# Kernel tuning notes

Hardware: AMD Instinct MI355X
Metric: run time of the kernel (lower is better)

Reference implementation:

```python
import jax, jax.numpy as jnp
import numpy as np

NUM_LAYERS = 4
INPUT_SIZE = 80
D_MODEL = 512
NHEAD = 8
D_FF = 2048
B = 16
S_MAX = 512
LN_EPS = 1e-5


def setup_inputs() -> dict:
    key = jax.random.key(0)
    ks = jax.random.split(key, 16)
    L, D, F, I = NUM_LAYERS, D_MODEL, D_FF, INPUT_SIZE
    s = 0.02
    inp = {
        "x": jax.random.normal(ks[0], (B, S_MAX, I), dtype=jnp.float32),
        "lens": jax.random.randint(ks[1], (B,), S_MAX // 2, S_MAX + 1, dtype=jnp.int32),
        "We": jax.random.normal(ks[2], (D, I), jnp.float32) * s,
        "be": jnp.zeros((D,), jnp.float32),
        "Wqkv": jax.random.normal(ks[3], (L, 3 * D, D), jnp.float32) * s,
        "bqkv": jnp.zeros((L, 3 * D), jnp.float32),
        "Wo": jax.random.normal(ks[4], (L, D, D), jnp.float32) * s,
        "bo": jnp.zeros((L, D), jnp.float32),
        "ln1_g": jnp.ones((L, D), jnp.float32),
        "ln1_b": jnp.zeros((L, D), jnp.float32),
        "W1": jax.random.normal(ks[5], (L, F, D), jnp.float32) * s,
        "b1": jnp.zeros((L, F), jnp.float32),
        "W2": jax.random.normal(ks[6], (L, D, F), jnp.float32) * s,
        "b2": jnp.zeros((L, D), jnp.float32),
        "ln2_g": jnp.ones((L, D), jnp.float32),
        "ln2_b": jnp.zeros((L, D), jnp.float32),
    }
    return inp


def _layer_norm(x, g, b):
    m = jnp.mean(x, axis=-1, keepdims=True)
    v = jnp.mean(jnp.square(x - m), axis=-1, keepdims=True)
    return (x - m) * jax.lax.rsqrt(v + LN_EPS) * g + b


def _pos_encoding(S, D, dtype):
    pos = jnp.arange(S, dtype=jnp.float32)[:, None]
    div = jnp.exp(jnp.arange(0, D, 2, dtype=jnp.float32) * (-np.log(10000.0) / D))
    pe = jnp.zeros((S, D), jnp.float32)
    pe = pe.at[:, 0::2].set(jnp.sin(pos * div))
    pe = pe.at[:, 1::2].set(jnp.cos(pos * div))
    return pe.astype(dtype)


def _encoder_layer(h, key_mask, Wqkv, bqkv, Wo, bo, g1, b1_, W1, b1f, W2, b2f, g2, b2_):
    # h: [B,S,D], key_mask: [B,S] bool (True = valid). Post-norm (PyTorch default).
    Bq, S, D = h.shape
    dh = D // NHEAD
    qkv = jnp.einsum("bsd,ed->bse", h, Wqkv) + bqkv  # [B,S,3D]
    q, k, v = jnp.split(qkv, 3, axis=-1)
    q = q.reshape(Bq, S, NHEAD, dh).transpose(0, 2, 1, 3)
    k = k.reshape(Bq, S, NHEAD, dh).transpose(0, 2, 1, 3)
    v = v.reshape(Bq, S, NHEAD, dh).transpose(0, 2, 1, 3)
    scores = jnp.einsum("bhqd,bhkd->bhqk", q, k) / jnp.sqrt(jnp.asarray(dh, h.dtype))
    scores = jnp.where(key_mask[:, None, None, :], scores, jnp.asarray(-1e9, h.dtype))
    attn = jax.nn.softmax(scores, axis=-1)
    ctx = jnp.einsum("bhqk,bhkd->bhqd", attn, v)
    ctx = ctx.transpose(0, 2, 1, 3).reshape(Bq, S, D)
    attn_out = jnp.einsum("bsd,ed->bse", ctx, Wo) + bo
    h = _layer_norm(h + attn_out, g1, b1_)
    ff = jnp.einsum("bsf,df->bsd", jax.nn.relu(jnp.einsum("bsd,fd->bsf", h, W1) + b1f), W2) + b2f
    return _layer_norm(h + ff, g2, b2_)


def reference(x, lens, We, be, Wqkv, bqkv, Wo, bo, ln1_g, ln1_b, W1, b1, W2, b2, ln2_g, ln2_b):
    Bq, S, _ = x.shape
    D = We.shape[0]
    h = jnp.einsum("bsi,di->bsd", x, We) + be  # Linear embedding
    h = h + _pos_encoding(S, D, h.dtype)[None]
    key_mask = jnp.arange(S)[None, :] < lens[:, None]  # [B,S]
    for l in range(Wqkv.shape[0]):
        h = _encoder_layer(h, key_mask, Wqkv[l], bqkv[l], Wo[l], bo[l],
                           ln1_g[l], ln1_b[l], W1[l], b1[l], W2[l], b2[l],
                           ln2_g[l], ln2_b[l])
    pooled = jnp.sum(h * key_mask[..., None].astype(h.dtype), axis=1)
    pooled = pooled / lens[:, None].astype(h.dtype)  # mean over valid tokens
    return pooled, lens
```

## Files before the change

kernel.cpp:

```cpp
#include <hip/hip_runtime.h>
#include <math.h>

#define D_MODEL 512
#define NHEAD   8
#define DH      64
#define D_FF    2048
#define BATCH   16
#define SMAX    512
#define NTOK    (BATCH*SMAX)
#define NLAYER  4

constexpr int MODE_QK   = 1;
constexpr int MODE_VT   = 2;
constexpr int MODE_RELU = 3;
constexpr int MODE_PART = 4;

typedef __attribute__((ext_vector_type(8))) __bf16 bf16x8;
typedef __attribute__((ext_vector_type(4))) float  f32x4;
typedef __attribute__((ext_vector_type(8))) int    i32x8;
typedef unsigned char u8;

#define WSCALE_INV 0.03125f
#define QSCALE     0.18033688011112042f

__device__ __forceinline__ unsigned short f2bf(float f) {
  union { float f; unsigned u; } v; v.f = f;
  unsigned r = v.u + 0x7FFFu + ((v.u >> 16) & 1u);
  return (unsigned short)(r >> 16);
}
__device__ __forceinline__ float bf2f(unsigned short u) {
  union { unsigned u; float f; } v; v.u = ((unsigned)u) << 16; return v.f;
}
__device__ __forceinline__ int pk4(float a, float b, float c, float d) {
  int t = __builtin_amdgcn_cvt_pk_fp8_f32(a, b, 0, false);
  t = __builtin_amdgcn_cvt_pk_fp8_f32(c, d, t, true);
  return t;
}

__device__ __forceinline__ void gl_lds16(const unsigned short* g, unsigned short* l) {
  __builtin_amdgcn_global_load_lds(
      (const __attribute__((address_space(1))) unsigned int*)g,
      (__attribute__((address_space(3)))       unsigned int*)l, 16, 0, 0);
}
__device__ __forceinline__ void gl_lds16b(const u8* g, u8* l) {
  __builtin_amdgcn_global_load_lds(
      (const __attribute__((address_space(1))) unsigned int*)g,
      (__attribute__((address_space(3)))       unsigned int*)l, 16, 0, 0);
}

__device__ __forceinline__ i32x8 ldfrag(const u8* base, int row, int q) {
  const int rx = row & 7;
  const int4 lo = *(const int4*)(base + (row << 7) + ((((2*q)    ) ^ rx) << 4));
  const int4 hi = *(const int4*)(base + (row << 7) + ((((2*q) + 1) ^ rx) << 4));
  union { int4 p[2]; i32x8 v; } u;
  u.p[0] = lo; u.p[1] = hi;
  return u.v;
}

template<int MODE>
__global__ __launch_bounds__(256)
void gemm_fp8(const u8* __restrict__ A, const u8* __restrict__ Bw,
              const float* __restrict__ bias, u8* __restrict__ C8,
              unsigned short* __restrict__ Cb,
              unsigned short* __restrict__ qd, unsigned short* __restrict__ kd,
              const int* __restrict__ lens, int K, int CK, int N)
{
  const int lin = blockIdx.x + gridDim.x*(blockIdx.y + gridDim.y*blockIdx.z);
  int m0, n0, kz = 0;
  {
    m0 = (lin % gridDim.y) * 128;
    const int rest = lin / gridDim.y;
    n0 = (rest % gridDim.x) * 128;
    kz = rest / gridDim.x;
  }
  if ((m0 & 511) >= lens[m0 >> 9]) return;

  __shared__ __attribute__((aligned(16))) u8 As[2][16384];
  __shared__ __attribute__((aligned(16))) u8 Bs[2][16384];
  const int tid  = threadIdx.x;
  const int lane = tid & 63;
  const int w    = tid >> 6;
  const int wm   = (w & 1) * 64;
  const int wn   = (w >> 1) * 64;
  const int l15  = lane & 15, quad = lane >> 4;

  f32x4 acc[4][4] = {};

  const int sr  = tid >> 3;
  const int sch = ((tid & 7) ^ (sr & 7)) * 16;
  const u8* Ag = A  + (long)(m0 + sr) * K + kz*CK + sch;
  const u8* Bg = Bw + (long)(n0 + sr) * K + kz*CK + sch;
  const long rowskip = (long)32 * K;
  const int t16 = tid * 16;
  const int niter = CK >> 7;

  auto stage = [&](int t, int bix) {
    const u8* a_ = Ag + t*128;
    const u8* b_ = Bg + t*128;
#pragma unroll
    for (int s = 0; s < 4; s++) {
      gl_lds16b(a_ + s*rowskip, &As[bix][s*4096 + t16]);
      gl_lds16b(b_ + s*rowskip, &Bs[bix][s*4096 + t16]);
    }
  };

  stage(0, 0);
  stage(1, 1);

  for (int it = 0; it < niter; ++it) {
    if (it + 1 < niter)
      asm volatile("s_waitcnt vmcnt(8)\n\ts_barrier" ::: "memory");
    else
      asm volatile("s_waitcnt vmcnt(0)\n\ts_barrier" ::: "memory");

    const int cur = it & 1;
    const u8* Ac = &As[cur][0];
    const u8* Bc = &Bs[cur][0];

    i32x8 bfv[4];
#pragma unroll
    for (int j = 0; j < 4; j++)
      bfv[j] = ldfrag(Bc, wn + j*16 + l15, quad);
#pragma unroll
    for (int i = 0; i < 4; i++) {
      const i32x8 af = ldfrag(Ac, wm + i*16 + l15, quad);
#pragma unroll
      for (int j = 0; j < 4; j++)
        acc[i][j] = __builtin_amdgcn_mfma_scale_f32_16x16x128_f8f6f4(
            af, bfv[j], acc[i][j], 0, 0, 0, 0x7F7F7F7F, 0, 0x7F7F7F7F);
    }

    if (it + 2 < niter) {
      __syncthreads();
      stage(it + 2, cur);
    }
  }

  __syncthreads();
  const int rr8 = lane >> 3, ch8 = lane & 7;

  if (MODE == MODE_RELU) {
    float* epf = (float*)&As[0][0] + w * 1088;
#pragma unroll
    for (int i = 0; i < 4; i++) {
#pragma unroll
      for (int j = 0; j < 4; j++) {
        const float cbv = bias[n0 + wn + j*16 + l15];
#pragma unroll
        for (int r = 0; r < 4; r++)
          epf[(quad*4 + r)*68 + j*16 + l15] = fmaxf(acc[i][j][r]*WSCALE_INV + cbv, 0.f);
      }
      asm volatile("s_waitcnt lgkmcnt(0)" ::: "memory");
      const int row = lane >> 2, c16 = (lane & 3) * 16;
      const float* rp = epf + row*68 + c16;
      f32x4 f0 = *(const f32x4*)(rp + 0);
      f32x4 f1 = *(const f32x4*)(rp + 4);
      f32x4 f2 = *(const f32x4*)(rp + 8);
      f32x4 f3 = *(const f32x4*)(rp + 12);
      int4 o;
      o.x = pk4(f0.x, f0.y, f0.z, f0.w);
      o.y = pk4(f1.x, f1.y, f1.z, f1.w);
      o.z = pk4(f2.x, f2.y, f2.z, f2.w);
      o.w = pk4(f3.x, f3.y, f3.z, f3.w);
      const int mrow = m0 + wm + i*16 + row;
      *(int4*)&C8[(long)mrow*N + n0 + wn + c16] = o;
      asm volatile("s_waitcnt lgkmcnt(0)" ::: "memory");
    }
  } else {
    unsigned short* epi = (unsigned short*)&As[0][0] + w * 1152;
#pragma unroll
    for (int i = 0; i < 4; i++) {
#pragma unroll
      for (int j = 0; j < 4; j++) {
#pragma unroll
        for (int r = 0; r < 4; r++) {
          float v = acc[i][j][r] * WSCALE_INV;
          epi[(quad*4 + r)*72 + j*16 + l15] = f2bf(v);
        }
      }
      asm volatile("s_waitcnt lgkmcnt(0)" ::: "memory");
#pragma unroll
      for (int rs = 0; rs < 2; rs++) {
        const int row  = rs*8 + rr8;
        const int mrow = m0 + wm + i*16 + row;
        bf16x8 val = *(const bf16x8*)&epi[row*72 + ch8*8];
        *(bf16x8*)&Cb[((long)kz*NTOK + mrow)*N + n0 + wn + ch8*8] = val;
      }
      asm volatile("s_waitcnt lgkmcnt(0)" ::: "memory");
    }
  }
}

__global__ __launch_bounds__(256)
void gemm_qkv(const u8* __restrict__ h8, const u8* __restrict__ wq,
              const float* __restrict__ bqkv,
              unsigned short* __restrict__ qd, unsigned short* __restrict__ kd,
              unsigned short* __restrict__ vt_b,
              const int* __restrict__ lens)
{
  const int lin = blockIdx.x;
  const bool isVT = lin >= 512;
  int m0, n0;
  if (isVT) { const int idx = lin - 512; n0 = (idx & 63) * 128; m0 = (idx >> 6) * 128; }
  else      { m0 = (lin & 63) * 128;     n0 = (lin >> 6) * 128; }
  { const int tb = isVT ? n0 : m0;
    if ((tb & 511) >= lens[tb >> 9]) return; }

  const u8* Ap = isVT ? (wq + (long)2*D_MODEL*D_MODEL) : h8;
  const u8* Bp = isVT ? h8 : wq;

  __shared__ __attribute__((aligned(16))) u8 As[2][16384];
  __shared__ __attribute__((aligned(16))) u8 Bs[2][16384];
  const int tid  = threadIdx.x;
  const int lane = tid & 63;
  const int w    = tid >> 6;
  const int wm   = (w & 1) * 64;
  const int wn   = (w >> 1) * 64;
  const int l15  = lane & 15, quad = lane >> 4;

  f32x4 acc[4][4] = {};

  const int sr  = tid >> 3;
  const int sch = ((tid & 7) ^ (sr & 7)) * 16;
  const u8* Ag = Ap + (long)(m0 + sr) * 512 + sch;
  const u8* Bg = Bp + (long)(n0 + sr) * 512 + sch;
  const long rowskip = (long)32 * 512;
  const int t16 = tid * 16;

  auto stage = [&](int t, int bix) {
    const u8* a_ = Ag + t*128;
    const u8* b_ = Bg + t*128;
#pragma unroll
    for (int s = 0; s < 4; s++) {
      gl_lds16b(a_ + s*rowskip, &As[bix][s*4096 + t16]);
      gl_lds16b(b_ + s*rowskip, &Bs[bix][s*4096 + t16]);
    }
  };

  stage(0, 0);
  stage(1, 1);

#pragma unroll 1
  for (int it = 0; it < 4; ++it) {
    if (it + 1 < 4)
      asm volatile("s_waitcnt vmcnt(8)\n\ts_barrier" ::: "memory");
    else
      asm volatile("s_waitcnt vmcnt(0)\n\ts_barrier" ::: "memory");

    const int cur = it & 1;
    const u8* Ac = &As[cur][0];
    const u8* Bc = &Bs[cur][0];

    i32x8 bfv[4];
#pragma unroll
    for (int j = 0; j < 4; j++)
      bfv[j] = ldfrag(Bc, wn + j*16 + l15, quad);
#pragma unroll
    for (int i = 0; i < 4; i++) {
      const i32x8 af = ldfrag(Ac, wm + i*16 + l15, quad);
#pragma unroll
      for (int j = 0; j < 4; j++)
        acc[i][j] = __builtin_amdgcn_mfma_scale_f32_16x16x128_f8f6f4(
            af, bfv[j], acc[i][j], 0, 0, 0, 0x7F7F7F7F, 0, 0x7F7F7F7F);
    }

    if (it + 2 < 4) {
      __syncthreads();
      stage(it + 2, cur);
    }
  }

  __syncthreads();
  const int rr8 = lane >> 3, ch8 = lane & 7;
  unsigned short* epi = (unsigned short*)&As[0][0] + w * 1152;
  const bool isq = !isVT && (((n0 + wn) >> 9) == 0);
#pragma unroll
  for (int i = 0; i < 4; i++) {
    float rbv[4];
    if (isVT) {
#pragma unroll
      for (int r = 0; r < 4; r++) rbv[r] = bqkv[2*D_MODEL + m0 + wm + i*16 + quad*4 + r];
    }
#pragma unroll
    for (int j = 0; j < 4; j++) {
      float cbv = 0.f;
      if (!isVT) cbv = bqkv[n0 + wn + j*16 + l15];
#pragma unroll
      for (int r = 0; r < 4; r++) {
        float v = acc[i][j][r] * WSCALE_INV;
        if (!isVT) { v += cbv; if (isq) v *= QSCALE; }
        else       v += rbv[r];
        epi[(quad*4 + r)*72 + j*16 + l15] = f2bf(v);
      }
    }
    asm volatile("s_waitcnt lgkmcnt(0)" ::: "memory");
#pragma unroll
    for (int rs = 0; rs < 2; rs++) {
      const int row  = rs*8 + rr8;
      const int mrow = m0 + wm + i*16 + row;
      bf16x8 val = *(const bf16x8*)&epi[row*72 + ch8*8];
      if (!isVT) {
        const int nb    = n0 + wn;
        const int which = nb >> 9;
        const int head  = (nb >> 6) & 7;
        unsigned short* dst = which ? kd : qd;
        const int bh = (mrow >> 9)*8 + head;
        *(bf16x8*)&dst[((long)(bh*512 + (mrow & 511)))*64 + ch8*8] = val;
      } else {
        const int head = mrow >> 6, d = mrow & 63;
        const int tok  = n0 + wn + ch8*8;
        const int b    = tok >> 9;
        *(bf16x8*)&vt_b[((long)((b*8 + head)*64 + d))*512 + (tok & 511)] = val;
      }
    }
    asm volatile("s_waitcnt lgkmcnt(0)" ::: "memory");
  }
}

template<int KS>
__global__ __launch_bounds__(128)
void reduce_ln(const unsigned short* __restrict__ part,
               const float* __restrict__ bias,
               const float* __restrict__ g, const float* __restrict__ bb,
               u8* __restrict__ h8, const int* __restrict__ lens)
{
  const int row = blockIdx.x, tid = threadIdx.x;
  if ((row & 511) >= lens[row >> 9]) return;
  const int hv = ((const int*)(h8 + (long)row*512))[tid];
  float4 bs = ((const float4*)bias)[tid];
  float v0 = __builtin_amdgcn_cvt_f32_fp8(hv, 0) + bs.x;
  float v1 = __builtin_amdgcn_cvt_f32_fp8(hv, 1) + bs.y;
  float v2 = __builtin_amdgcn_cvt_f32_fp8(hv, 2) + bs.z;
  float v3 = __builtin_amdgcn_cvt_f32_fp8(hv, 3) + bs.w;
#pragma unroll
  for (int z = 0; z < KS; z++) {
    ushort4 p = ((const ushort4*)(part + ((long)z*NTOK + row)*512))[tid];
    v0 += bf2f(p.x); v1 += bf2f(p.y); v2 += bf2f(p.z); v3 += bf2f(p.w);
  }
  float s  = v0 + v1 + v2 + v3;
  float s2 = v0*v0 + v1*v1 + v2*v2 + v3*v3;
#pragma unroll
  for (int off = 1; off < 64; off <<= 1) {
    s  += __shfl_xor(s, off);
    s2 += __shfl_xor(s2, off);
  }
  __shared__ float rb[4];
  if ((tid & 63) == 0) { rb[(tid>>6)*2] = s; rb[(tid>>6)*2+1] = s2; }
  __syncthreads();
  s = rb[0] + rb[2]; s2 = rb[1] + rb[3];
  const float mean = s * (1.f/512.f);
  const float var  = fmaxf(s2 * (1.f/512.f) - mean*mean, 0.f);
  const float rstd = rsqrtf(var + 1e-5f);
  const int e = tid*4;
  const float o0 = (v0-mean)*rstd*g[e+0] + bb[e+0];
  const float o1 = (v1-mean)*rstd*g[e+1] + bb[e+1];
  const float o2 = (v2-mean)*rstd*g[e+2] + bb[e+2];
  const float o3 = (v3-mean)*rstd*g[e+3] + bb[e+3];
  ((int*)(h8 + (long)row*512))[tid] = pk4(o0, o1, o2, o3);
}

__global__ __launch_bounds__(256)
void attn_mfma(const unsigned short* __restrict__ qg,
               const unsigned short* __restrict__ kb,
               const unsigned short* __restrict__ vtb,
               const int* __restrict__ lens,
               u8* __restrict__ ctx8)
{
  const int bh = blockIdx.x, qt = blockIdx.y;
  const int b = bh >> 3, hh = bh & 7;
  const int len = lens[b];
  if (qt*64 >= len) return;

  __shared__ __attribute__((aligned(16))) u8 smem[41984];
  unsigned short* Ks0 = (unsigned short*)smem;
  unsigned short* Vts0 = (unsigned short*)(smem + 16384);
  unsigned short* Ps  = (unsigned short*)(smem + 32768);
  const int tid = threadIdx.x;
  const int w = tid >> 6, lane = tid & 63, l15 = lane & 15, quad = lane >> 4;
  const int t8 = tid * 8;

  const int srow = tid >> 2;
  const int s8   = (tid & 3) * 8;
  const unsigned short* Kbase = kb  + ((long)(bh*512 + srow))*64 + s8;
  const unsigned short* Vbase = vtb + ((long)(bh*64 + srow))*512 + s8;

  const unsigned short* qrow = qg + ((long)(bh*512 + qt*64 + w*16 + l15))*64;
  const bf16x8 qf0 = *(const bf16x8*)(qrow + quad*8);
  const bf16x8 qf1 = *(const bf16x8*)(qrow + 32 + quad*8);

  f32x4 O[4] = {};
  float lrow[4] = {0.f,0.f,0.f,0.f};
  unsigned short* Pw = &Ps[w*16*72];
  const int ntiles = (len + 63) >> 6;

  {
    gl_lds16(Kbase,      &Ks0[t8]);
    gl_lds16(Kbase + 32, &Ks0[2048 + t8]);
    gl_lds16(Vbase,      &Vts0[t8]);
    gl_lds16(Vbase + 32, &Vts0[2048 + t8]);
  }

  for (int kt = 0; kt < ntiles; kt++) {
    const int cur = kt & 1;
    unsigned short* Kc  = Ks0  + cur*4096;
    unsigned short* Vc  = Vts0 + cur*4096;
    __syncthreads();
    if (kt + 1 < ntiles) {
      const unsigned short* Kg = Kbase + (long)(kt+1)*64*64;
      const unsigned short* Vg = Vbase + (long)(kt+1)*64;
      unsigned short* Kn = Ks0  + (cur^1)*4096;
      unsigned short* Vn = Vts0 + (cur^1)*4096;
      gl_lds16(Kg,      &Kn[t8]);
      gl_lds16(Kg + 32, &Kn[2048 + t8]);
      gl_lds16(Vg,      &Vn[t8]);
      gl_lds16(Vg + 32, &Vn[2048 + t8]);
    }

    f32x4 sc[4];
#pragma unroll
    for (int ks = 0; ks < 4; ks++) {
      bf16x8 kf0 = *(const bf16x8*)&Kc[       (ks*16 + l15)*32 + quad*8];
      bf16x8 kf1 = *(const bf16x8*)&Kc[2048 + (ks*16 + l15)*32 + quad*8];
      f32x4 z = {};
      z = __builtin_amdgcn_mfma_f32_16x16x32_bf16(qf0, kf0, z, 0, 0, 0);
      sc[ks] = __builtin_amdgcn_mfma_f32_16x16x32_bf16(qf1, kf1, z, 0, 0, 0);
    }

    if (kt*64 + 64 > len) {
#pragma unroll
      for (int ks = 0; ks < 4; ks++) {
        const bool valid = (kt*64 + ks*16 + l15) < len;
#pragma unroll
        for (int r = 0; r < 4; r++)
          sc[ks][r] = valid ? sc[ks][r] : -1e30f;
      }
    }

    float pv[4][4];
#pragma unroll
    for (int ks = 0; ks < 4; ks++)
#pragma unroll
      for (int r = 0; r < 4; r++) {
        const float p = exp2f(sc[ks][r] - 16.f);
        pv[ks][r] = p;
        lrow[r] += p;
      }

#pragma unroll
    for (int ks = 0; ks < 4; ks++)
#pragma unroll
      for (int r = 0; r < 4; r++)
        Pw[(quad*4 + r)*72 + ks*16 + l15] = f2bf(pv[ks][r]);
    asm volatile("s_waitcnt lgkmcnt(0)" ::: "memory");

    const bf16x8 pa0 = *(const bf16x8*)&Pw[l15*72 + quad*8];
    const bf16x8 pa1 = *(const bf16x8*)&Pw[l15*72 + 32 + quad*8];
#pragma unroll
    for (int d = 0; d < 4; d++) {
      bf16x8 vf0 = *(const bf16x8*)&Vc[       (d*16 + l15)*32 + quad*8];
      bf16x8 vf1 = *(const bf16x8*)&Vc[2048 + (d*16 + l15)*32 + quad*8];
      O[d] = __builtin_amdgcn_mfma_f32_16x16x32_bf16(pa0, vf0, O[d], 0, 0, 0);
      O[d] = __builtin_amdgcn_mfma_f32_16x16x32_bf16(pa1, vf1, O[d], 0, 0, 0);
    }
  }

#pragma unroll
  for (int r = 0; r < 4; r++) {
    float t = lrow[r];
    t += __shfl_xor(t, 1);
    t += __shfl_xor(t, 2);
    t += __shfl_xor(t, 4);
    t += __shfl_xor(t, 8);
    lrow[r] = t;
  }

  __syncthreads();
  float* epf = (float*)smem + w * 1088;
#pragma unroll
  for (int r = 0; r < 4; r++) {
    const float inv = 1.f / lrow[r];
#pragma unroll
    for (int d = 0; d < 4; d++)
      epf[(quad*4 + r)*68 + d*16 + l15] = O[d][r] * inv;
  }
  asm volatile("s_waitcnt lgkmcnt(0)" ::: "memory");
  {
    const int row = lane >> 2, c16 = (lane & 3) * 16;
    const float* rp = epf + row*68 + c16;
    f32x4 f0 = *(const f32x4*)(rp + 0);
    f32x4 f1 = *(const f32x4*)(rp + 4);
    f32x4 f2 = *(const f32x4*)(rp + 8);
    f32x4 f3 = *(const f32x4*)(rp + 12);
    int4 o;
    o.x = pk4(f0.x, f0.y, f0.z, f0.w);
    o.y = pk4(f1.x, f1.y, f1.z, f1.w);
    o.z = pk4(f2.x, f2.y, f2.z, f2.w);
    o.w = pk4(f3.x, f3.y, f3.z, f3.w);
    const long gaddr = (long)(b*512 + qt*64 + w*16 + row)*512 + hh*64 + c16;
    *(int4*)&ctx8[gaddr] = o;
  }
}

__global__ __launch_bounds__(256)
void gemm_embed(const float* __restrict__ A, const float* __restrict__ Bm,
                const float* __restrict__ bias,
                u8* __restrict__ C8, int K, int N)
{
  __shared__ float As[8][132];
  __shared__ float Bs[8][68];
  const int tid = threadIdx.x;
  const int m0 = blockIdx.y * 128;
  const int n0 = blockIdx.x * 64;
  const int tx = tid & 15, ty = tid >> 4;
  const int a_k = tid & 7, a_m = tid >> 3;

  float acc[8][4] = {};
  const float* Ag = A  + (long)(m0 + a_m) * K + a_k;
  const float* Bg = Bm + (long)(n0 + a_m) * K + a_k;

  for (int k0 = 0; k0 < K; k0 += 8) {
#pragma unroll
    for (int i = 0; i < 4; i++)
      As[a_k][a_m + 32*i] = Ag[k0 + (long)32*i*K];
#pragma unroll
    for (int i = 0; i < 2; i++)
      Bs[a_k][a_m + 32*i] = Bg[k0 + (long)32*i*K];
    __syncthreads();
#pragma unroll
    for (int kk = 0; kk < 8; kk++) {
      float a[8], bv[4];
#pragma unroll
      for (int r = 0; r < 8; r++) a[r] = As[kk][ty*8 + r];
#pragma unroll
      for (int c = 0; c < 4; c++) bv[c] = Bs[kk][tx*4 + c];
#pragma unroll
      for (int r = 0; r < 8; r++)
#pragma unroll
        for (int c = 0; c < 4; c++)
          acc[r][c] += a[r] * bv[c];
    }
    __syncthreads();
  }

  const int n_base = n0 + tx*4;
  const float cfreq = -13.287712379549449f / 512.0f;
  const float dv0 = exp2f((float)(n_base)     * cfreq);
  const float dv1 = exp2f((float)(n_base + 2) * cfreq);
#pragma unroll
  for (int r = 0; r < 8; r++) {
    int m = m0 + ty*8 + r;
    int s = m & 511;
    float a0 = (float)s * dv0, a1 = (float)s * dv1;
    float s0v, c0v, s1v, c1v;
    __sincosf(a0, &s0v, &c0v);
    __sincosf(a1, &s1v, &c1v);
    int o = pk4(acc[r][0] + bias[n_base+0] + s0v,
                acc[r][1] + bias[n_base+1] + c0v,
                acc[r][2] + bias[n_base+2] + s1v,
                acc[r][3] + bias[n_base+3] + c1v);
    *(int*)(C8 + (long)m*N + n_base) = o;
  }
}

#define N4_QKV (NLAYER*3*D_MODEL*D_MODEL/4)
#define N4_WO  (NLAYER*D_MODEL*D_MODEL/4)
#define N4_W1  (NLAYER*D_FF*D_MODEL/4)
#define N4_W2  (NLAYER*D_MODEL*D_FF/4)
__global__ __launch_bounds__(256)
void cvt_all(const float* __restrict__ wq, const float* __restrict__ wo,
             const float* __restrict__ w1, const float* __restrict__ w2,
             u8* __restrict__ oq, u8* __restrict__ oo,
             u8* __restrict__ o1, u8* __restrict__ o2)
{
  int i = blockIdx.x*256 + threadIdx.x;
  const float* src; u8* dst; int off;
  if (i < N4_QKV)                          { src = wq; dst = oq; off = i; }
  else if (i < N4_QKV + N4_WO)             { src = wo; dst = oo; off = i - N4_QKV; }
  else if (i < N4_QKV + N4_WO + N4_W1)     { src = w1; dst = o1; off = i - N4_QKV - N4_WO; }
  else if (i < N4_QKV + N4_WO + N4_W1 + N4_W2) { src = w2; dst = o2; off = i - N4_QKV - N4_WO - N4_W1; }
  else return;
  float4 v = ((const float4*)src)[off];
  ((int*)dst)[off] = pk4(v.x*32.f, v.y*32.f, v.z*32.f, v.w*32.f);
}

__global__ __launch_bounds__(256)
void out_init(float* __restrict__ out, const int* __restrict__ lens)
{
  int i = blockIdx.x*256 + threadIdx.x;
  if (i < 8192) out[i] = 0.f;
  else if (i < 8192 + 16) out[i] = (float)lens[i - 8192];
}

__global__ __launch_bounds__(256)
void pool_kernel(const u8* __restrict__ h8,
                 const int* __restrict__ lens, float* __restrict__ out)
{
  const int b = blockIdx.y;
  const int s0 = blockIdx.x * 64;
  const int len = lens[b];
  if (s0 >= len) return;
  const int send = min(s0 + 64, len);
  const int tid = threadIdx.x;
  const int c = (tid & 127) * 4;
  const int half = tid >> 7;
  float a0 = 0.f, a1 = 0.f, a2 = 0.f, a3 = 0.f;
  for (int s = s0 + half; s < send; s += 2) {
    const int v = *(const int*)(h8 + ((long)(b*512 + s))*512 + c);
    a0 += __builtin_amdgcn_cvt_f32_fp8(v, 0);
    a1 += __builtin_amdgcn_cvt_f32_fp8(v, 1);
    a2 += __builtin_amdgcn_cvt_f32_fp8(v, 2);
    a3 += __builtin_amdgcn_cvt_f32_fp8(v, 3);
  }
  const float inv = 1.0f / (float)len;
  atomicAdd(out + b*512 + c + 0, a0 * inv);
  atomicAdd(out + b*512 + c + 1, a1 * inv);
  atomicAdd(out + b*512 + c + 2, a2 * inv);
  atomicAdd(out + b*512 + c + 3, a3 * inv);
}

extern "C" void kernel_launch(void* const* d_in, const int* in_sizes, int n_in,
                              void* d_out, int out_size, void* d_ws, size_t ws_size,
                              hipStream_t stream)
{
  const float* x    = (const float*)d_in[0];
  const int*   lens = (const int*)  d_in[1];
  const float* We   = (const float*)d_in[2];
  const float* be   = (const float*)d_in[3];
  const float* Wqkv = (const float*)d_in[4];
  const float* bqkv = (const float*)d_in[5];
  const float* Wo   = (const float*)d_in[6];
  const float* bo   = (const float*)d_in[7];
  const float* ln1g = (const float*)d_in[8];
  const float* ln1b = (const float*)d_in[9];
  const float* W1   = (const float*)d_in[10];
  const float* b1   = (const float*)d_in[11];
  const float* W2   = (const float*)d_in[12];
  const float* b2   = (const float*)d_in[13];
  const float* ln2g = (const float*)d_in[14];
  const float* ln2b = (const float*)d_in[15];
  float* out = (float*)d_out;

  const long TOK_D = (long)NTOK * D_MODEL;
  u8* base = (u8*)d_ws;
  u8* h8    = base + 4*TOK_D;
  u8* ctx8  = h8   + TOK_D;
  u8* ff8   = ctx8 + TOK_D;
  unsigned short* q_b  = (unsigned short*)(ff8 + 4*TOK_D);
  unsigned short* k_b  = q_b + TOK_D;
  unsigned short* vt_b = k_b + TOK_D;
  unsigned short* part = vt_b + TOK_D;
  u8* wq8 = (u8*)(part + 4*TOK_D);
  u8* wo8 = wq8 + (long)NLAYER*3*D_MODEL*D_MODEL;
  u8* w18 = wo8 + (long)NLAYER*D_MODEL*D_MODEL;
  u8* w28 = w18 + (long)NLAYER*D_FF*D_MODEL;

  const dim3 blk(256);

  {
    const int n4tot = N4_QKV + N4_WO + N4_W1 + N4_W2;
    cvt_all<<<dim3((n4tot+255)/256), blk, 0, stream>>>(
        Wqkv, Wo, W1, W2, wq8, wo8, w18, w28);
  }

  gemm_embed<<<dim3(D_MODEL/64, NTOK/128), blk, 0, stream>>>(
      x, We, be, h8, 80, D_MODEL);

  for (int l = 0; l < NLAYER; l++) {
    const u8* wq_l = wq8 + (long)l * 3*D_MODEL * D_MODEL;
    const u8* wo_l = wo8 + (long)l * D_MODEL * D_MODEL;
    const u8* w1_l = w18 + (long)l * D_FF * D_MODEL;
    const u8* w2_l = w28 + (long)l * D_MODEL * D_FF;
    const float* bqkv_l = bqkv + (long)l * 3*D_MODEL;
    const float* bo_l   = bo   + (long)l * D_MODEL;
    const float* b1_l   = b1   + (long)l * D_FF;
    const float* b2_l   = b2   + (long)l * D_MODEL;

    gemm_qkv<<<dim3(768), blk, 0, stream>>>(
        h8, wq_l, bqkv_l, q_b, k_b, vt_b, lens);

    attn_mfma<<<dim3(NHEAD*BATCH, SMAX/64), blk, 0, stream>>>(
        q_b, k_b, vt_b, lens, ctx8);

    gemm_fp8<MODE_PART><<<dim3(D_MODEL/128, NTOK/128, 2), blk, 0, stream>>>(
        ctx8, wo_l, nullptr, nullptr, part, nullptr, nullptr, lens,
        D_MODEL, D_MODEL/2, D_MODEL);
    reduce_ln<2><<<dim3(NTOK), dim3(128), 0, stream>>>(
        part, bo_l, ln1g + l*D_MODEL, ln1b + l*D_MODEL, h8, lens);

    gemm_fp8<MODE_RELU><<<dim3(D_FF/128, NTOK/128), blk, 0, stream>>>(
        h8, w1_l, b1_l, ff8, nullptr, nullptr, nullptr, lens, D_MODEL, D_MODEL, D_FF);

    gemm_fp8<MODE_PART><<<dim3(D_MODEL/128, NTOK/128, 2), blk, 0, stream>>>(
        ff8, w2_l, nullptr, nullptr, part, nullptr, nullptr, lens,
        D_FF, D_FF/2, D_MODEL);
    reduce_ln<2><<<dim3(NTOK), dim3(128), 0, stream>>>(
        part, b2_l, ln2g + l*D_MODEL, ln2b + l*D_MODEL, h8, lens);
  }

  out_init<<<dim3((8192 + 16 + 255) / 256), blk, 0, stream>>>(out, lens);
  pool_kernel<<<dim3(SMAX/64, BATCH), blk, 0, stream>>>(h8, lens, out);
}
```

Before: 495.3 us.

## Load B fragments directly from global into registers, halving GEMM LDS use

In both fp8 GEMM kernels the B (weight/activation) tile is no longer staged through LDS; each lane reads its MFMA fragment straight from global memory into registers, double-buffered across two unrolled iterations with adjusted vmcnt waits. This halves shared memory per block, which can raise occupancy, and removes the LDS reads for B, at the cost of uncoalesced 32-byte global loads and more live registers. Separately, the out_init and atomic pool kernels are merged into one per-batch pooling kernel that reduces in LDS and writes the output directly.

```diff
diff --git a/kernel.cpp b/kernel.cpp
--- a/kernel.cpp
+++ b/kernel.cpp
@@ -10,8 +10,6 @@
 #define NTOK    (BATCH*SMAX)
 #define NLAYER  4
 
-constexpr int MODE_QK   = 1;
-constexpr int MODE_VT   = 2;
 constexpr int MODE_RELU = 3;
 constexpr int MODE_PART = 4;
 
@@ -57,12 +55,19 @@
   return u.v;
 }
 
+__device__ __forceinline__ i32x8 ldBg(const u8* p) {
+  const int4 lo = *(const int4*)(p);
+  const int4 hi = *(const int4*)(p + 16);
+  union { int4 p2[2]; i32x8 v; } u;
+  u.p2[0] = lo; u.p2[1] = hi;
+  return u.v;
+}
+
 template<int MODE>
 __global__ __launch_bounds__(256)
 void gemm_fp8(const u8* __restrict__ A, const u8* __restrict__ Bw,
               const float* __restrict__ bias, u8* __restrict__ C8,
               unsigned short* __restrict__ Cb,
-              unsigned short* __restrict__ qd, unsigned short* __restrict__ kd,
               const int* __restrict__ lens, int K, int CK, int N)
 {
   const int lin = blockIdx.x + gridDim.x*(blockIdx.y + gridDim.y*blockIdx.z);
@@ -76,7 +81,6 @@
   if ((m0 & 511) >= lens[m0 >> 9]) return;
 
   __shared__ __attribute__((aligned(16))) u8 As[2][16384];
-  __shared__ __attribute__((aligned(16))) u8 Bs[2][16384];
   const int tid  = threadIdx.x;
   const int lane = tid & 63;
   const int w    = tid >> 6;
@@ -89,51 +93,67 @@
   const int sr  = tid >> 3;
   const int sch = ((tid & 7) ^ (sr & 7)) * 16;
   const u8* Ag = A  + (long)(m0 + sr) * K + kz*CK + sch;
-  const u8* Bg = Bw + (long)(n0 + sr) * K + kz*CK + sch;
   const long rowskip = (long)32 * K;
   const int t16 = tid * 16;
   const int niter = CK >> 7;
 
-  auto stage = [&](int t, int bix) {
+  const u8* Bgl = Bw + (long)(n0 + wn + l15) * K + kz*CK + quad*32;
+  const long rk16 = (long)16 * K;
+
+  auto stageA = [&](int t, int bix) {
     const u8* a_ = Ag + t*128;
-    const u8* b_ = Bg + t*128;
-#pragma unroll
-    for (int s = 0; s < 4; s++) {
+#pragma unroll
+    for (int s = 0; s < 4; s++)
       gl_lds16b(a_ + s*rowskip, &As[bix][s*4096 + t16]);
-      gl_lds16b(b_ + s*rowskip, &Bs[bix][s*4096 + t16]);
-    }
   };
 
-  stage(0, 0);
-  stage(1, 1);
-
-  for (int it = 0; it < niter; ++it) {
-    if (it + 1 < niter)
-      asm volatile("s_waitcnt vmcnt(8)\n\ts_barrier" ::: "memory");
-    else
-      asm volatile("s_waitcnt vmcnt(0)\n\ts_barrier" ::: "memory");
-
-    const int cur = it & 1;
-    const u8* Ac = &As[cur][0];
-    const u8* Bc = &Bs[cur][0];
-
-    i32x8 bfv[4];
-#pragma unroll
-    for (int j = 0; j < 4; j++)
-      bfv[j] = ldfrag(Bc, wn + j*16 + l15, quad);
-#pragma unroll
-    for (int i = 0; i < 4; i++) {
-      const i32x8 af = ldfrag(Ac, wm + i*16 + l15, quad);
-#pragma unroll
-      for (int j = 0; j < 4; j++)
-        acc[i][j] = __builtin_amdgcn_mfma_scale_f32_16x16x128_f8f6f4(
-            af, bfv[j], acc[i][j], 0, 0, 0, 0x7F7F7F7F, 0, 0x7F7F7F7F);
-    }
-
-    if (it + 2 < niter) {
-      __syncthreads();
-      stage(it + 2, cur);
-    }
+  i32x8 bA[4], bB[4];
+  auto loadB = [&](int t, i32x8* dst) {
+    const u8* p = Bgl + (long)t * 128;
+    dst[0] = ldBg(p);
+    dst[1] = ldBg(p + rk16);
+    dst[2] = ldBg(p + 2*rk16);
+    dst[3] = ldBg(p + 3*rk16);
+  };
+
+  stageA(0, 0);
+  stageA(1, 1);
+  asm volatile("" ::: "memory");
+  loadB(0, bA);
+
+  for (int it = 0; it < niter; it += 2) {
+    if (it + 1 < niter) asm volatile("s_waitcnt vmcnt(12)\n\ts_barrier" ::: "memory");
+    else                asm volatile("s_waitcnt vmcnt(0)\n\ts_barrier" ::: "memory");
+    if (it + 1 < niter) loadB(it + 1, bB);
+    {
+      const u8* Ac = &As[it & 1][0];
+#pragma unroll
+      for (int i = 0; i < 4; i++) {
+        const i32x8 af = ldfrag(Ac, wm + i*16 + l15, quad);
+#pragma unroll
+        for (int j = 0; j < 4; j++)
+          acc[i][j] = __builtin_amdgcn_mfma_scale_f32_16x16x128_f8f6f4(
+              af, bA[j], acc[i][j], 0, 0, 0, 0x7F7F7F7F, 0, 0x7F7F7F7F);
+      }
+    }
+    if (it + 2 < niter) { __syncthreads(); stageA(it + 2, it & 1); }
+
+    const int it2 = it + 1;
+    if (it2 + 1 < niter) asm volatile("s_waitcnt vmcnt(12)\n\ts_barrier" ::: "memory");
+    else                 asm volatile("s_waitcnt vmcnt(0)\n\ts_barrier" ::: "memory");
+    if (it2 + 1 < niter) loadB(it2 + 1, bA);
+    {
+      const u8* Ac = &As[it2 & 1][0];
+#pragma unroll
+      for (int i = 0; i < 4; i++) {
+        const i32x8 af = ldfrag(Ac, wm + i*16 + l15, quad);
+#pragma unroll
+        for (int j = 0; j < 4; j++)
+          acc[i][j] = __builtin_amdgcn_mfma_scale_f32_16x16x128_f8f6f4(
+              af, bB[j], acc[i][j], 0, 0, 0, 0x7F7F7F7F, 0, 0x7F7F7F7F);
+      }
+    }
+    if (it2 + 2 < niter) { __syncthreads(); stageA(it2 + 2, it2 & 1); }
   }
 
   __syncthreads();
@@ -210,7 +230,6 @@
   const u8* Bp = isVT ? h8 : wq;
 
   __shared__ __attribute__((aligned(16))) u8 As[2][16384];
-  __shared__ __attribute__((aligned(16))) u8 Bs[2][16384];
   const int tid  = threadIdx.x;
   const int lane = tid & 63;
   const int w    = tid >> 6;
@@ -223,51 +242,67 @@
   const int sr  = tid >> 3;
   const int sch = ((tid & 7) ^ (sr & 7)) * 16;
   const u8* Ag = Ap + (long)(m0 + sr) * 512 + sch;
-  const u8* Bg = Bp + (long)(n0 + sr) * 512 + sch;
   const long rowskip = (long)32 * 512;
   const int t16 = tid * 16;
 
-  auto stage = [&](int t, int bix) {
+  const u8* Bgl = Bp + (long)(n0 + wn + l15) * 512 + quad*32;
+  const long rk16 = (long)16 * 512;
+
+  auto stageA = [&](int t, int bix) {
     const u8* a_ = Ag + t*128;
-    const u8* b_ = Bg + t*128;
-#pragma unroll
-    for (int s = 0; s < 4; s++) {
+#pragma unroll
+    for (int s = 0; s < 4; s++)
       gl_lds16b(a_ + s*rowskip, &As[bix][s*4096 + t16]);
-      gl_lds16b(b_ + s*rowskip, &Bs[bix][s*4096 + t16]);
-    }
   };
 
-  stage(0, 0);
-  stage(1, 1);
+  i32x8 bA[4], bB[4];
+  auto loadB = [&](int t, i32x8* dst) {
+    const u8* p = Bgl + (long)t * 128;
+    dst[0] = ldBg(p);
+    dst[1] = ldBg(p + rk16);
+    dst[2] = ldBg(p + 2*rk16);
+    dst[3] = ldBg(p + 3*rk16);
+  };
+
+  stageA(0, 0);
+  stageA(1, 1);
+  asm volatile("" ::: "memory");
+  loadB(0, bA);
 
 #pragma unroll 1
-  for (int it = 0; it < 4; ++it) {
-    if (it + 1 < 4)
-      asm volatile("s_waitcnt vmcnt(8)\n\ts_barrier" ::: "memory");
-    else
-      asm volatile("s_waitcnt vmcnt(0)\n\ts_barrier" ::: "memory");
-
-    const int cur = it & 1;
-    const u8* Ac = &As[cur][0];
-    const u8* Bc = &Bs[cur][0];
-
-    i32x8 bfv[4];
-#pragma unroll
-    for (int j = 0; j < 4; j++)
-      bfv[j] = ldfrag(Bc, wn + j*16 + l15, quad);
-#pragma unroll
-    for (int i = 0; i < 4; i++) {
-      const i32x8 af = ldfrag(Ac, wm + i*16 + l15, quad);
-#pragma unroll
-      for (int j = 0; j < 4; j++)
-        acc[i][j] = __builtin_amdgcn_mfma_scale_f32_16x16x128_f8f6f4(
-            af, bfv[j], acc[i][j], 0, 0, 0, 0x7F7F7F7F, 0, 0x7F7F7F7F);
-    }
-
-    if (it + 2 < 4) {
-      __syncthreads();
-      stage(it + 2, cur);
-    }
+  for (int it = 0; it < 4; it += 2) {
+    if (it + 1 < 4) asm volatile("s_waitcnt vmcnt(12)\n\ts_barrier" ::: "memory");
+    else            asm volatile("s_waitcnt vmcnt(0)\n\ts_barrier" ::: "memory");
+    if (it + 1 < 4) loadB(it + 1, bB);
+    {
+      const u8* Ac = &As[it & 1][0];
+#pragma unroll
+      for (int i = 0; i < 4; i++) {
+        const i32x8 af = ldfrag(Ac, wm + i*16 + l15, quad);
+#pragma unroll
+        for (int j = 0; j < 4; j++)
+          acc[i][j] = __builtin_amdgcn_mfma_scale_f32_16x16x128_f8f6f4(
+              af, bA[j], acc[i][j], 0, 0, 0, 0x7F7F7F7F, 0, 0x7F7F7F7F);
+      }
+    }
+    if (it + 2 < 4) { __syncthreads(); stageA(it + 2, it & 1); }
+
+    const int it2 = it + 1;
+    if (it2 + 1 < 4) asm volatile("s_waitcnt vmcnt(12)\n\ts_barrier" ::: "memory");
+    else             asm volatile("s_waitcnt vmcnt(0)\n\ts_barrier" ::: "memory");
+    if (it2 + 1 < 4) loadB(it2 + 1, bA);
+    {
+      const u8* Ac = &As[it2 & 1][0];
+#pragma unroll
+      for (int i = 0; i < 4; i++) {
+        const i32x8 af = ldfrag(Ac, wm + i*16 + l15, quad);
+#pragma unroll
+        for (int j = 0; j < 4; j++)
+          acc[i][j] = __builtin_amdgcn_mfma_scale_f32_16x16x128_f8f6f4(
+              af, bB[j], acc[i][j], 0, 0, 0, 0x7F7F7F7F, 0, 0x7F7F7F7F);
+      }
+    }
+    if (it2 + 2 < 4) { __syncthreads(); stageA(it2 + 2, it2 & 1); }
   }
 
   __syncthreads();
@@ -584,38 +619,35 @@
 }
 
 __global__ __launch_bounds__(256)
-void out_init(float* __restrict__ out, const int* __restrict__ lens)
+void pool_one(const u8* __restrict__ h8,
+              const int* __restrict__ lens, float* __restrict__ out)
 {
-  int i = blockIdx.x*256 + threadIdx.x;
-  if (i < 8192) out[i] = 0.f;
-  else if (i < 8192 + 16) out[i] = (float)lens[i - 8192];
-}
-
-__global__ __launch_bounds__(256)
-void pool_kernel(const u8* __restrict__ h8,
-                 const int* __restrict__ lens, float* __restrict__ out)
-{
-  const int b = blockIdx.y;
-  const int s0 = blockIdx.x * 64;
+  const int b = blockIdx.x;
   const int len = lens[b];
-  if (s0 >= len) return;
-  const int send = min(s0 + 64, len);
   const int tid = threadIdx.x;
   const int c = (tid & 127) * 4;
   const int half = tid >> 7;
   float a0 = 0.f, a1 = 0.f, a2 = 0.f, a3 = 0.f;
-  for (int s = s0 + half; s < send; s += 2) {
+  for (int s = half; s < len; s += 2) {
     const int v = *(const int*)(h8 + ((long)(b*512 + s))*512 + c);
     a0 += __builtin_amdgcn_cvt_f32_fp8(v, 0);
     a1 += __builtin_amdgcn_cvt_f32_fp8(v, 1);
     a2 += __builtin_amdgcn_cvt_f32_fp8(v, 2);
     a3 += __builtin_amdgcn_cvt_f32_fp8(v, 3);
   }
-  const float inv = 1.0f / (float)len;
-  atomicAdd(out + b*512 + c + 0, a0 * inv);
-  atomicAdd(out + b*512 + c + 1, a1 * inv);
-  atomicAdd(out + b*512 + c + 2, a2 * inv);
-  atomicAdd(out + b*512 + c + 3, a3 * inv);
+  __shared__ float buf[512];
+  if (half) {
+    buf[c+0] = a0; buf[c+1] = a1; buf[c+2] = a2; buf[c+3] = a3;
+  }
+  __syncthreads();
+  if (!half) {
+    const float inv = 1.0f / (float)len;
+    out[b*512 + c + 0] = (a0 + buf[c+0]) * inv;
+    out[b*512 + c + 1] = (a1 + buf[c+1]) * inv;
+    out[b*512 + c + 2] = (a2 + buf[c+2]) * inv;
+    out[b*512 + c + 3] = (a3 + buf[c+3]) * inv;
+  }
+  if (b == 0 && tid < 16) out[8192 + tid] = (float)lens[tid];
 }
 
 extern "C" void kernel_launch(void* const* d_in, const int* in_sizes, int n_in,
@@ -682,21 +714,20 @@
         q_b, k_b, vt_b, lens, ctx8);
 
     gemm_fp8<MODE_PART><<<dim3(D_MODEL/128, NTOK/128, 2), blk, 0, stream>>>(
-        ctx8, wo_l, nullptr, nullptr, part, nullptr, nullptr, lens,
+        ctx8, wo_l, nullptr, nullptr, part, lens,
         D_MODEL, D_MODEL/2, D_MODEL);
     reduce_ln<2><<<dim3(NTOK), dim3(128), 0, stream>>>(
         part, bo_l, ln1g + l*D_MODEL, ln1b + l*D_MODEL, h8, lens);
 
     gemm_fp8<MODE_RELU><<<dim3(D_FF/128, NTOK/128), blk, 0, stream>>>(
-        h8, w1_l, b1_l, ff8, nullptr, nullptr, nullptr, lens, D_MODEL, D_MODEL, D_FF);
+        h8, w1_l, b1_l, ff8, nullptr, lens, D_MODEL, D_MODEL, D_FF);
 
     gemm_fp8<MODE_PART><<<dim3(D_MODEL/128, NTOK/128, 2), blk, 0, stream>>>(
-        ff8, w2_l, nullptr, nullptr, part, nullptr, nullptr, lens,
+        ff8, w2_l, nullptr, nullptr, part, lens,
         D_FF, D_FF/2, D_MODEL);
     reduce_ln<2><<<dim3(NTOK), dim3(128), 0, stream>>>(
         part, b2_l, ln2g + l*D_MODEL, ln2b + l*D_MODEL, h8, lens);
   }
 
-  out_init<<<dim3((8192 + 16 + 255) / 256), blk, 0, stream>>>(out, lens);
-  pool_kernel<<<dim3(SMAX/64, BATCH), blk, 0, stream>>>(h8, lens, out);
-}
+  pool_one<<<dim3(BATCH), blk, 0, stream>>>(h8, lens, out);
+}
```

After: 781.5 us. +57.8%, slower.
